# Optimization experiments

Hardware: AMD Instinct MI355X
Metric: run time of the kernel (lower is better)

The kernel has to match this reference:

```python
import math
import jax, jax.numpy as jnp
import numpy as np

B, S, E = 2, 2048, 2048
H, D = 16, 128

def setup_inputs() -> dict:
    key = jax.random.key(0)
    ks = jax.random.split(key, 5)
    scale = 0.02
    return {
        "hidden_states": jax.random.normal(ks[0], (B, S, E), dtype=jnp.float32),
        "Wq": jax.random.normal(ks[1], (E, E), dtype=jnp.float32) * scale,
        "Wk": jax.random.normal(ks[2], (E, E), dtype=jnp.float32) * scale,
        "Wv": jax.random.normal(ks[3], (E, E), dtype=jnp.float32) * scale,
        "Wo": jax.random.normal(ks[4], (E, E), dtype=jnp.float32) * scale,
        "bo": jnp.zeros((E,), dtype=jnp.float32),
    }

def _split_heads(x):
    # [B,S,E] -> [B,H,S,D]
    b, s, _ = x.shape
    return x.reshape(b, s, H, D).transpose(0, 2, 1, 3)

def reference(hidden_states, Wq, Wk, Wv, Wo, bo):
    # torch nn.Linear: y = x @ W.T (q/k/v have no bias)
    q = _split_heads(hidden_states @ Wq.T)
    k = _split_heads(hidden_states @ Wk.T)
    v = _split_heads(hidden_states @ Wv.T)
    scores = jnp.einsum("bhqd,bhkd->bhqk", q, k) / math.sqrt(D)
    # causal mask: strictly-upper-triangular positions set to -inf ...
    causal = jnp.triu(jnp.ones((S, S), dtype=bool), k=1)
    scores = jnp.where(causal[None, None], -jnp.inf, scores)
    # ... then clamped to [-1e4, 1e4] (so masked logits become -10000, not -inf)
    scores = jnp.clip(scores, -10000.0, 10000.0)
    attn = jax.nn.softmax(scores, axis=-1)
    out = jnp.einsum("bhqk,bhkd->bhqd", attn, v)  # [B,H,S,D]
    out = out.transpose(0, 2, 1, 3).reshape(B, S, E)  # merge heads
    return out @ Wo.T + bo
```

## Files before the change

kernel.cpp:

```cpp
#include <hip/hip_runtime.h>
#include <hip/hip_bf16.h>
#include <stdint.h>
#include <math.h>

#define B_ 2
#define S_ 2048
#define E_ 2048
#define H_ 16
#define D_ 128
#define M_ (B_*S_)

#define QSCALE 0.1275174308f

typedef _Float16 half8 __attribute__((ext_vector_type(8)));
typedef _Float16 half4 __attribute__((ext_vector_type(4)));
typedef float    floatx4 __attribute__((ext_vector_type(4)));

__device__ __forceinline__ void async_copy16(const void* g, void* lds_base) {
    __builtin_amdgcn_global_load_lds(
        (__attribute__((address_space(1))) void*)(uintptr_t)g,
        (__attribute__((address_space(3))) void*)(uint32_t)(uintptr_t)lds_base,
        16, 0, 0);
}

template<int CTRL>
__device__ __forceinline__ float dpp_mv(float x) {
    return __int_as_float(__builtin_amdgcn_update_dpp(
        0, __float_as_int(x), CTRL, 0xF, 0xF, true));
}
__device__ __forceinline__ float row_max16(float x) {
    x = fmaxf(x, dpp_mv<0xB1>(x));
    x = fmaxf(x, dpp_mv<0x4E>(x));
    x = fmaxf(x, dpp_mv<0x124>(x));
    x = fmaxf(x, dpp_mv<0x128>(x));
    return x;
}
__device__ __forceinline__ float row_sum16(float x) {
    x += dpp_mv<0xB1>(x);
    x += dpp_mv<0x4E>(x);
    x += dpp_mv<0x124>(x);
    x += dpp_mv<0x128>(x);
    return x;
}
__device__ __forceinline__ float fexp2(float x) {
    float r; __asm__("v_exp_f32 %0, %1" : "=v"(r) : "v"(x)); return r;
}

__global__ __launch_bounds__(256) void cast_all(
    const float* __restrict__ X,  const float* __restrict__ Wq,
    const float* __restrict__ Wk, const float* __restrict__ Wv,
    const float* __restrict__ Wo,
    _Float16* __restrict__ Xh,  _Float16* __restrict__ Wqh,
    _Float16* __restrict__ Wkh, _Float16* __restrict__ Wvh,
    _Float16* __restrict__ Woh)
{
    const int z = blockIdx.z;
    const float* in; _Float16* out; size_t off = 0;
    switch (z) {
        case 0: in = X;  out = Xh;  off = 0;        break;
        case 1: in = X;  out = Xh;  off = 1048576;  break;
        case 2: in = Wq; out = Wqh; break;
        case 3: in = Wk; out = Wkh; break;
        case 4: in = Wv; out = Wvh; break;
        default: in = Wo; out = Woh; break;
    }
    size_t i = off + (size_t)blockIdx.x * 256 + threadIdx.x;
    floatx4 v = ((const floatx4*)in)[i];
    ((half4*)out)[i] = __builtin_convertvector(v, half4);
}

#define GBUF (128*64 + 128*64)

__device__ __forceinline__ void stage512(
    const _Float16* __restrict__ gsrc, int ldk,
    _Float16* lbase, int slot0, int wave, int lane)
{
    int slot = slot0 + wave*64 + lane;
    int row  = slot >> 3;
    int sg   = (slot & 7) ^ (row & 7);
    async_copy16(gsrc + (size_t)row * ldk + sg * 8,
                 lbase + (slot0 + wave*64) * 8);
}

template<bool BIAS, typename OutT, int NW, bool TRV>
__global__ __launch_bounds__(256, 2) void gemm_bt(
    const _Float16* __restrict__ A,
    const _Float16* __restrict__ W0, const _Float16* __restrict__ W1,
    const _Float16* __restrict__ W2,
    OutT* __restrict__ C0, OutT* __restrict__ C1, OutT* __restrict__ C2,
    const float* __restrict__ bias, int M, int N, int K)
{
    const _Float16* W = W0; OutT* C = C0;
    if (NW > 1) {
        if (blockIdx.y == 1) { W = W1; C = C1; }
        else if (blockIdx.y == 2) { W = W2; C = C2; }
    }
    __shared__ __align__(16) _Float16 sm[2 * GBUF];

    const int tid  = threadIdx.x;
    const int lane = tid & 63;
    const int wave = tid >> 6;
    const int wm = wave >> 1, wn = wave & 1;
    const int fr = lane & 15, fg = lane >> 4;

    const int bx = blockIdx.x;
    const int n_tile = bx & 15;
    const int m_tile = bx >> 4;
    const int m0 = m_tile * 128;
    const int n0 = n_tile * 128;

    const int NT = K >> 6;

    {
        _Float16* ab = &sm[0];
        _Float16* bb = ab + 128*64;
        const _Float16* Ag = A + (size_t)m0 * K;
        const _Float16* Wg = W + (size_t)n0 * K;
#pragma unroll
        for (int s0 = 0; s0 < 1024; s0 += 256) {
            stage512(Ag, K, ab, s0, wave, lane);
            stage512(Wg, K, bb, s0, wave, lane);
        }
    }

    floatx4 acc[4][4] = {};

    for (int t = 0; t < NT; ++t) {
        __asm__ __volatile__("s_waitcnt vmcnt(0)" ::: "memory");
        __builtin_amdgcn_sched_barrier(0);
        __builtin_amdgcn_s_barrier();
        __builtin_amdgcn_sched_barrier(0);

        const _Float16* Ab = &sm[(t & 1) * GBUF];
        const _Float16* Bb = Ab + 128*64;

        if (t + 1 < NT) {
            _Float16* pab = &sm[((t + 1) & 1) * GBUF];
            _Float16* pbb = pab + 128*64;
            const _Float16* pAg = A + (size_t)m0 * K + (t + 1)*64;
            const _Float16* pWg = W + (size_t)n0 * K + (t + 1)*64;
#pragma unroll
            for (int s0 = 0; s0 < 1024; s0 += 256) {
                stage512(pAg, K, pab, s0, wave, lane);
                stage512(pWg, K, pbb, s0, wave, lane);
            }
        }

        half8 af[4][2], bf[4][2];
#pragma unroll
        for (int mt = 0; mt < 4; ++mt)
#pragma unroll
            for (int kk = 0; kk < 2; ++kk) {
                int row = wm*64 + mt*16 + fr;
                int g = (kk*4 + fg) ^ (row & 7);
                af[mt][kk] = *(const half8*)&Ab[row*64 + g*8];
            }
#pragma unroll
        for (int nt = 0; nt < 4; ++nt)
#pragma unroll
            for (int kk = 0; kk < 2; ++kk) {
                int row = wn*64 + nt*16 + fr;
                int g = (kk*4 + fg) ^ (row & 7);
                bf[nt][kk] = *(const half8*)&Bb[row*64 + g*8];
            }

        __builtin_amdgcn_s_setprio(1);
#pragma unroll
        for (int kk = 0; kk < 2; ++kk)
#pragma unroll
            for (int nt = 0; nt < 4; ++nt)
#pragma unroll
                for (int mt = 0; mt < 4; ++mt)
                    acc[mt][nt] = __builtin_amdgcn_mfma_f32_16x16x32_f16(
                        af[mt][kk], bf[nt][kk], acc[mt][nt], 0, 0, 0);
        __builtin_amdgcn_s_setprio(0);
    }

    if (TRV && NW > 1 && blockIdx.y == 2) {
        _Float16* Vt = (_Float16*)C;
#pragma unroll
        for (int mt = 0; mt < 4; ++mt)
#pragma unroll
            for (int nt = 0; nt < 4; ++nt) {
                int col  = n0 + wn*64 + nt*16 + fr;
                int row0 = m0 + wm*64 + mt*16 + fg*4;
                int bq = row0 >> 11, s0 = row0 & 2047;
                int hq = col >> 7,  dq = col & 127;
                half4 v;
#pragma unroll
                for (int r = 0; r < 4; ++r) v[r] = (_Float16)acc[mt][nt][r];
                *(half4*)&Vt[(((size_t)(bq*16 + hq) * 128 + dq) << 11) + s0] = v;
            }
    } else {
        const float qs = (NW > 1 && blockIdx.y == 0) ? QSCALE : 1.f;
#pragma unroll
        for (int mt = 0; mt < 4; ++mt)
#pragma unroll
            for (int nt = 0; nt < 4; ++nt) {
                int col = n0 + wn*64 + nt*16 + fr;
                float bv = BIAS ? bias[col] : 0.f;
#pragma unroll
                for (int r = 0; r < 4; ++r) {
                    int row = m0 + wm*64 + mt*16 + fg*4 + r;
                    C[(size_t)row * N + col] = (OutT)(acc[mt][nt][r] * qs + bv);
                }
            }
    }
}

__global__ __launch_bounds__(256, 2) void attn_causal_coop(
    const _Float16* __restrict__ Q, const _Float16* __restrict__ K,
    const _Float16* __restrict__ Vt, _Float16* __restrict__ O)
{
    const int n   = blockIdx.x;
    const int xcd = n & 7;
    const int idx = n >> 3;
    const int bh  = xcd * 4 + (idx >> 4);
    const int j   = idx & 15;
    const int b = bh >> 4, h = bh & 15;
    const int tid = threadIdx.x, lane = tid & 63, wave = tid >> 6;
    const int fr = lane & 15, fg = lane >> 4;

    __shared__ __align__(16) _Float16 Ks[64*128];
    __shared__ __align__(16) _Float16 Vs[128*64];
    __shared__ __align__(16) _Float16 Ps[4][32*72];

    const int rhi = (31 - j) * 64 + wave * 16;
    const int rlo = j * 64 + wave * 16;
    const int nkt = 32 - j;

    half8 qf[2][4];
    {
        const _Float16* qb0 = Q + ((size_t)(b*S_) + rhi) * E_ + h*D_;
        const _Float16* qb1 = Q + ((size_t)(b*S_) + rlo) * E_ + h*D_;
#pragma unroll
        for (int kk = 0; kk < 4; ++kk) {
            qf[0][kk] = *(const half8*)&qb0[(size_t)fr * E_ + kk*32 + fg*8];
            qf[1][kk] = *(const half8*)&qb1[(size_t)fr * E_ + kk*32 + fg*8];
        }
    }

    float m_i[2][4], l_i[2][4];
    floatx4 o[2][8] = {};
#pragma unroll
    for (int mt = 0; mt < 2; ++mt)
#pragma unroll
        for (int r = 0; r < 4; ++r) { m_i[mt][r] = -INFINITY; l_i[mt][r] = 0.f; }

    const _Float16* kg = K + (size_t)(b*S_) * E_ + h*D_;
    const _Float16* vg = Vt + (size_t)bh * D_ * S_;
    _Float16* ps = &Ps[wave][0];

    for (int jt = 0; jt < nkt; ++jt) {
        __syncthreads();
#pragma unroll
        for (int q = 0; q < 4; ++q) {
            int G = q*256 + tid;
            int row = G >> 4, slot = G & 15;
            int c = slot ^ (row & 7);
            async_copy16(kg + (size_t)(jt*64 + row) * E_ + c*8,
                         &Ks[(q*256 + wave*64) * 8]);
        }
#pragma unroll
        for (int q = 0; q < 4; ++q) {
            int G = q*256 + tid;
            int row = G >> 3, slot = G & 7;
            int c = slot ^ (row & 7);
            async_copy16(vg + (size_t)row * S_ + jt*64 + c*8,
                         &Vs[(q*256 + wave*64) * 8]);
        }
        __syncthreads();

        const bool lo_act = (jt <= j);

        floatx4 sacc[2][4] = {};
#pragma unroll
        for (int kk = 0; kk < 4; ++kk) {
            half8 bf[4];
#pragma unroll
            for (int nt = 0; nt < 4; ++nt)
                bf[nt] = *(const half8*)
                    &Ks[(nt*16 + fr)*128 + (((kk*4 + fg) ^ (fr & 7)) * 8)];
#pragma unroll
            for (int nt = 0; nt < 4; ++nt)
                sacc[0][nt] = __builtin_amdgcn_mfma_f32_16x16x32_f16(
                    qf[0][kk], bf[nt], sacc[0][nt], 0, 0, 0);
            if (lo_act) {
#pragma unroll
                for (int nt = 0; nt < 4; ++nt)
                    sacc[1][nt] = __builtin_amdgcn_mfma_f32_16x16x32_f16(
                        qf[1][kk], bf[nt], sacc[1][nt], 0, 0, 0);
            }
        }

        const int kc0 = jt*64 + fr;
#pragma unroll
        for (int mt = 0; mt < 2; ++mt) {
            if (mt == 1 && !lo_act) continue;
            const bool diag = mt ? (jt == j) : (jt == nkt - 1);
            const int qr0 = (mt ? rlo : rhi) + fg*4;
            float alpha[4];
#pragma unroll
            for (int r = 0; r < 4; ++r) {
                float mx;
                if (diag) {
                    mx = -INFINITY;
#pragma unroll
                    for (int nt = 0; nt < 4; ++nt) {
                        float s = sacc[mt][nt][r];
                        s = (kc0 + nt*16 <= qr0 + r) ? s : -INFINITY;
                        sacc[mt][nt][r] = s;
                        mx = fmaxf(mx, s);
                    }
                } else {
                    mx = fmaxf(fmaxf(sacc[mt][0][r], sacc[mt][1][r]),
                               fmaxf(sacc[mt][2][r], sacc[mt][3][r]));
                }
                mx = row_max16(mx);
                float mnew = fmaxf(m_i[mt][r], mx);
                alpha[r] = (m_i[mt][r] == -INFINITY) ? 0.f : fexp2(m_i[mt][r] - mnew);
                float rs = 0.f;
#pragma unroll
                for (int nt = 0; nt < 4; ++nt) {
                    float p = fexp2(sacc[mt][nt][r] - mnew);
                    sacc[mt][nt][r] = p;
                    rs += p;
                }
                rs = row_sum16(rs);
                l_i[mt][r] = alpha[r] * l_i[mt][r] + rs;
                m_i[mt][r] = mnew;
            }
#pragma unroll
            for (int dt = 0; dt < 8; ++dt)
#pragma unroll
                for (int r = 0; r < 4; ++r) o[mt][dt][r] *= alpha[r];

#pragma unroll
            for (int nt = 0; nt < 4; ++nt)
#pragma unroll
                for (int r = 0; r < 4; ++r)
                    ps[(mt*16 + fg*4 + r)*72 + nt*16 + fr] = (_Float16)sacc[mt][nt][r];
        }
        __asm__ __volatile__("s_waitcnt lgkmcnt(0)" ::: "memory");
        __builtin_amdgcn_sched_barrier(0);

#pragma unroll
        for (int kk = 0; kk < 2; ++kk) {
            half8 pf0 = *(const half8*)&ps[(fr)*72 + kk*32 + fg*8];
            half8 pf1 = *(const half8*)&ps[(16 + fr)*72 + kk*32 + fg*8];
#pragma unroll
            for (int dt = 0; dt < 8; ++dt) {
                half8 vf = *(const half8*)
                    &Vs[(dt*16 + fr)*64 + (((kk*4 + fg) ^ (fr & 7)) * 8)];
                o[0][dt] = __builtin_amdgcn_mfma_f32_16x16x32_f16(
                    pf0, vf, o[0][dt], 0, 0, 0);
                if (lo_act)
                    o[1][dt] = __builtin_amdgcn_mfma_f32_16x16x32_f16(
                        pf1, vf, o[1][dt], 0, 0, 0);
            }
        }
    }

#pragma unroll
    for (int mt = 0; mt < 2; ++mt) {
        const int rbase = mt ? rlo : rhi;
        _Float16* ob = O + ((size_t)(b*S_) + rbase) * E_ + h*D_;
#pragma unroll
        for (int r = 0; r < 4; ++r) {
            float inv = 1.f / l_i[mt][r];
#pragma unroll
            for (int dt = 0; dt < 8; ++dt)
                ob[(size_t)(fg*4 + r) * E_ + dt*16 + fr] = (_Float16)(o[mt][dt][r] * inv);
        }
    }
}

extern "C" void kernel_launch(void* const* d_in, const int* in_sizes, int n_in,
                              void* d_out, int out_size, void* d_ws, size_t ws_size,
                              hipStream_t stream) {
    const float* X  = (const float*)d_in[0];
    const float* Wq = (const float*)d_in[1];
    const float* Wk = (const float*)d_in[2];
    const float* Wv = (const float*)d_in[3];
    const float* Wo = (const float*)d_in[4];
    const float* bo = (const float*)d_in[5];
    float* out = (float*)d_out;

    const size_t ME = (size_t)M_ * E_;
    const size_t EE = (size_t)E_ * E_;
    _Float16* ws  = (_Float16*)d_ws;
    _Float16* Xh  = ws;
    _Float16* Wqh = Xh  + ME;
    _Float16* Wkh = Wqh + EE;
    _Float16* Wvh = Wkh + EE;
    _Float16* Woh = Wvh + EE;
    _Float16* Qh  = Woh + EE;
    _Float16* Kh  = Qh  + ME;
    _Float16* Vth = Kh  + ME;
    _Float16* Oh  = Xh;

    cast_all<<<dim3(4096, 1, 6), dim3(256), 0, stream>>>(
        X, Wq, Wk, Wv, Wo, Xh, Wqh, Wkh, Wvh, Woh);

    gemm_bt<false, _Float16, 3, true><<<dim3(512, 3), dim3(256), 0, stream>>>(
        Xh, Wqh, Wkh, Wvh, Qh, Kh, Vth, nullptr, M_, E_, E_);

    attn_causal_coop<<<dim3(512), dim3(256), 0, stream>>>(Qh, Kh, Vth, Oh);

    gemm_bt<true, float, 1, false><<<dim3(512, 1), dim3(256), 0, stream>>>(
        Oh, Woh, nullptr, nullptr, out, nullptr, nullptr, bo, M_, E_, E_);
}
```

Measured before the change: 368.1 us.

## Double-buffer K/V tiles, add lazy softmax rescaling, swizzle P LDS layout

The attention kernel now double-buffers the K and V tiles in LDS, prefetching tile jt+1 while tile jt is computed. This replaces the two __syncthreads per iteration with a single vmcnt wait and barrier. It also skips the online-softmax rescale of O and l unless some row's max grows by more than 8 (log2 units), which saves exp and multiply work on most tiles. The P scratch buffer changes from padded stride 72 to an XOR-swizzled stride 64 layout. The trade-off is doubled K/V LDS use, which may lower occupancy from the 2 blocks requested, and lazy rescaling allows exponents up to 2^8 before correction, which risks fp16 overflow in P.

Measured after the change: 368.3 us. No clear change (+0.0%).

```diff
diff --git a/kernel.cpp b/kernel.cpp
--- a/kernel.cpp
+++ b/kernel.cpp
@@ -221,9 +221,9 @@
     const int tid = threadIdx.x, lane = tid & 63, wave = tid >> 6;
     const int fr = lane & 15, fg = lane >> 4;
 
-    __shared__ __align__(16) _Float16 Ks[64*128];
-    __shared__ __align__(16) _Float16 Vs[128*64];
-    __shared__ __align__(16) _Float16 Ps[4][32*72];
+    __shared__ __align__(16) _Float16 Ks[2][64*128];
+    __shared__ __align__(16) _Float16 Vs[2][128*64];
+    __shared__ __align__(16) _Float16 Ps[4][32*64];
 
     const int rhi = (31 - j) * 64 + wave * 16;
     const int rlo = j * 64 + wave * 16;
@@ -251,27 +251,43 @@
     const _Float16* vg = Vt + (size_t)bh * D_ * S_;
     _Float16* ps = &Ps[wave][0];
 
+#pragma unroll
+    for (int q = 0; q < 4; ++q) {
+        int G = q*256 + tid;
+        { int row = G >> 4, slot = G & 15;
+          int c = slot ^ (row & 7);
+          async_copy16(kg + (size_t)row * E_ + c*8, &Ks[0][(q*256 + wave*64) * 8]); }
+        { int row = G >> 3, slot = G & 7;
+          int c = slot ^ (row & 7);
+          async_copy16(vg + (size_t)row * S_ + c*8, &Vs[0][(q*256 + wave*64) * 8]); }
+    }
+
     for (int jt = 0; jt < nkt; ++jt) {
-        __syncthreads();
-#pragma unroll
-        for (int q = 0; q < 4; ++q) {
-            int G = q*256 + tid;
-            int row = G >> 4, slot = G & 15;
-            int c = slot ^ (row & 7);
-            async_copy16(kg + (size_t)(jt*64 + row) * E_ + c*8,
-                         &Ks[(q*256 + wave*64) * 8]);
-        }
-#pragma unroll
-        for (int q = 0; q < 4; ++q) {
-            int G = q*256 + tid;
-            int row = G >> 3, slot = G & 7;
-            int c = slot ^ (row & 7);
-            async_copy16(vg + (size_t)row * S_ + jt*64 + c*8,
-                         &Vs[(q*256 + wave*64) * 8]);
-        }
-        __syncthreads();
+        __asm__ __volatile__("s_waitcnt vmcnt(0)" ::: "memory");
+        __builtin_amdgcn_sched_barrier(0);
+        __builtin_amdgcn_s_barrier();
+        __builtin_amdgcn_sched_barrier(0);
+
+        const int cur = jt & 1, nxt = cur ^ 1;
+
+        if (jt + 1 < nkt) {
+#pragma unroll
+            for (int q = 0; q < 4; ++q) {
+                int G = q*256 + tid;
+                { int row = G >> 4, slot = G & 15;
+                  int c = slot ^ (row & 7);
+                  async_copy16(kg + (size_t)((jt+1)*64 + row) * E_ + c*8,
+                               &Ks[nxt][(q*256 + wave*64) * 8]); }
+                { int row = G >> 3, slot = G & 7;
+                  int c = slot ^ (row & 7);
+                  async_copy16(vg + (size_t)row * S_ + (jt+1)*64 + c*8,
+                               &Vs[nxt][(q*256 + wave*64) * 8]); }
+            }
+        }
 
         const bool lo_act = (jt <= j);
+        const _Float16* kt = &Ks[cur][0];
+        const _Float16* vt = &Vs[cur][0];
 
         floatx4 sacc[2][4] = {};
 #pragma unroll
@@ -280,7 +296,7 @@
 #pragma unroll
             for (int nt = 0; nt < 4; ++nt)
                 bf[nt] = *(const half8*)
-                    &Ks[(nt*16 + fr)*128 + (((kk*4 + fg) ^ (fr & 7)) * 8)];
+                    &kt[(nt*16 + fr)*128 + (((kk*4 + fg) ^ (fr & 7)) * 8)];
 #pragma unroll
             for (int nt = 0; nt < 4; ++nt)
                 sacc[0][nt] = __builtin_amdgcn_mfma_f32_16x16x32_f16(
@@ -299,59 +315,79 @@
             if (mt == 1 && !lo_act) continue;
             const bool diag = mt ? (jt == j) : (jt == nkt - 1);
             const int qr0 = (mt ? rlo : rhi) + fg*4;
-            float alpha[4];
+            float mx[4];
 #pragma unroll
             for (int r = 0; r < 4; ++r) {
-                float mx;
+                float m0v;
                 if (diag) {
-                    mx = -INFINITY;
+                    m0v = -INFINITY;
 #pragma unroll
                     for (int nt = 0; nt < 4; ++nt) {
                         float s = sacc[mt][nt][r];
                         s = (kc0 + nt*16 <= qr0 + r) ? s : -INFINITY;
                         sacc[mt][nt][r] = s;
-                        mx = fmaxf(mx, s);
+                        m0v = fmaxf(m0v, s);
                     }
                 } else {
-                    mx = fmaxf(fmaxf(sacc[mt][0][r], sacc[mt][1][r]),
-                               fmaxf(sacc[mt][2][r], sacc[mt][3][r]));
+                    m0v = fmaxf(fmaxf(sacc[mt][0][r], sacc[mt][1][r]),
+                                fmaxf(sacc[mt][2][r], sacc[mt][3][r]));
                 }
-                mx = row_max16(mx);
-                float mnew = fmaxf(m_i[mt][r], mx);
-                alpha[r] = (m_i[mt][r] == -INFINITY) ? 0.f : fexp2(m_i[mt][r] - mnew);
+                mx[r] = row_max16(m0v);
+            }
+            bool grow = false;
+#pragma unroll
+            for (int r = 0; r < 4; ++r)
+                grow = grow || (mx[r] > m_i[mt][r] + 8.f);
+            if (__any(grow)) {
+                float alpha[4];
+#pragma unroll
+                for (int r = 0; r < 4; ++r) {
+                    float mnew = fmaxf(m_i[mt][r], mx[r]);
+                    alpha[r] = (m_i[mt][r] == -INFINITY) ? 0.f
+                                                         : fexp2(m_i[mt][r] - mnew);
+                    l_i[mt][r] *= alpha[r];
+                    m_i[mt][r] = mnew;
+                }
+#pragma unroll
+                for (int dt = 0; dt < 8; ++dt)
+#pragma unroll
+                    for (int r = 0; r < 4; ++r) o[mt][dt][r] *= alpha[r];
+            }
+#pragma unroll
+            for (int r = 0; r < 4; ++r) {
                 float rs = 0.f;
 #pragma unroll
                 for (int nt = 0; nt < 4; ++nt) {
-                    float p = fexp2(sacc[mt][nt][r] - mnew);
+                    float p = fexp2(sacc[mt][nt][r] - m_i[mt][r]);
                     sacc[mt][nt][r] = p;
                     rs += p;
                 }
                 rs = row_sum16(rs);
-                l_i[mt][r] = alpha[r] * l_i[mt][r] + rs;
-                m_i[mt][r] = mnew;
-            }
-#pragma unroll
-            for (int dt = 0; dt < 8; ++dt)
-#pragma unroll
-                for (int r = 0; r < 4; ++r) o[mt][dt][r] *= alpha[r];
-
+                l_i[mt][r] += rs;
+            }
 #pragma unroll
             for (int nt = 0; nt < 4; ++nt)
 #pragma unroll
-                for (int r = 0; r < 4; ++r)
-                    ps[(mt*16 + fg*4 + r)*72 + nt*16 + fr] = (_Float16)sacc[mt][nt][r];
+                for (int r = 0; r < 4; ++r) {
+                    int q  = mt*16 + fg*4 + r;
+                    int gl = nt*2 + (fr >> 3);
+                    ps[q*64 + ((gl ^ (q & 7)) << 3) + (fr & 7)]
+                        = (_Float16)sacc[mt][nt][r];
+                }
         }
         __asm__ __volatile__("s_waitcnt lgkmcnt(0)" ::: "memory");
         __builtin_amdgcn_sched_barrier(0);
 
 #pragma unroll
         for (int kk = 0; kk < 2; ++kk) {
-            half8 pf0 = *(const half8*)&ps[(fr)*72 + kk*32 + fg*8];
-            half8 pf1 = *(const half8*)&ps[(16 + fr)*72 + kk*32 + fg*8];
+            half8 pf0 = *(const half8*)
+                &ps[(fr)*64 + (((kk*4 + fg) ^ (fr & 7)) << 3)];
+            half8 pf1 = *(const half8*)
+                &ps[(16 + fr)*64 + (((kk*4 + fg) ^ (fr & 7)) << 3)];
 #pragma unroll
             for (int dt = 0; dt < 8; ++dt) {
                 half8 vf = *(const half8*)
-                    &Vs[(dt*16 + fr)*64 + (((kk*4 + fg) ^ (fr & 7)) * 8)];
+                    &vt[(dt*16 + fr)*64 + (((kk*4 + fg) ^ (fr & 7)) * 8)];
                 o[0][dt] = __builtin_amdgcn_mfma_f32_16x16x32_f16(
                     pf0, vf, o[0][dt], 0, 0, 0);
                 if (lo_act)
```
